# Kernel optimization log

Hardware: AMD Instinct MI355X
Metric: run time of the kernel (lower is better)

## Reference

```python
import jax, jax.numpy as jnp
import numpy as np

N, C_IN, C_OUT, K_CHEB, BATCH = 2048, 64, 64, 4, 8


def setup_inputs() -> dict:
    key = jax.random.key(0)
    k1, k2, k3, k4, k5 = jax.random.split(key, 5)
    # Xavier-uniform-like scales
    s_nn = float(np.sqrt(6.0 / (N + N)))
    s_th = float(np.sqrt(6.0 / (C_IN + C_OUT)))
    return {
        "X": jax.random.normal(k1, (BATCH, N, C_IN), dtype=jnp.float32),
        "Ws": jax.random.uniform(k2, (N, N), jnp.float32, -s_nn, s_nn),
        "W_alpha": jax.random.uniform(k3, (N, N), jnp.float32, -s_nn, s_nn),
        "Theta_s": jax.random.uniform(k4, (K_CHEB, C_IN, C_OUT), jnp.float32, -s_th, s_th),
        "Theta_d": jax.random.uniform(k5, (K_CHEB, C_IN, C_OUT), jnp.float32, -s_th, s_th),
    }


def reference(X, Ws, W_alpha, Theta_s, Theta_d):
    B, n, c_in = X.shape
    K = Theta_s.shape[0]

    # ---- static filter: sum_k (T_k(Ws) @ X) @ Theta_s[k] ----
    # T_0 = I, so T_0 @ X = X
    static_filter = jnp.einsum('bni,io->bno', X, Theta_s[0])
    if K > 1:
        T_prev2 = jnp.eye(n, dtype=X.dtype)
        T_prev1 = Ws  # T_1
        for k in range(1, K):
            TkX = jnp.einsum('nm,bmi->bni', T_prev1, X)
            static_filter = static_filter + jnp.einsum('bni,io->bno', TkX, Theta_s[k])
            if k + 1 < K:  # incremental Chebyshev recursion (same values as from-scratch)
                T_prev2, T_prev1 = T_prev1, 2.0 * (Ws @ T_prev1) - T_prev2

    # ---- dynamic filter ----
    # Wd = X @ (W_alpha @ X)^T  -> [B, n, n]
    WaX = jnp.einsum('nm,bmi->bni', W_alpha, X)
    Wd = jnp.einsum('bni,bmi->bnm', X, WaX)

    dynamic_filter = jnp.einsum('bni,io->bno', X, Theta_d[0])
    if K > 1:
        Td_prev2 = jnp.broadcast_to(jnp.eye(n, dtype=X.dtype), (B, n, n))
        Td_prev1 = Wd  # T_1
        for k in range(1, K):
            TkX = jnp.einsum('bnm,bmi->bni', Td_prev1, X)
            dynamic_filter = dynamic_filter + jnp.einsum('bni,io->bno', TkX, Theta_d[k])
            if k + 1 < K:
                Td_prev2, Td_prev1 = Td_prev1, 2.0 * jnp.matmul(Wd, Td_prev1) - Td_prev2

    return jax.nn.relu(static_filter) + jax.nn.relu(dynamic_filter)
```

## Files before the change

### kernel.cpp

```cpp
#include <hip/hip_runtime.h>

typedef __attribute__((ext_vector_type(8))) short bf16x8;
typedef __attribute__((ext_vector_type(4))) float f32x4;

__device__ __forceinline__ ushort f32_to_bf16(float f) {
    union { float f; unsigned u; } v; v.f = f;
    unsigned b = v.u + 0x7FFF + ((v.u >> 16) & 1);
    return (ushort)(b >> 16);
}
__device__ __forceinline__ float bf16_to_f32(ushort h) {
    union { unsigned u; float f; } v; v.u = ((unsigned)h) << 16;
    return v.f;
}
__device__ __forceinline__ void split2(float x, ushort& a, ushort& b) {
    a = f32_to_bf16(x); float r1 = x - bf16_to_f32(a);
    b = f32_to_bf16(r1);
}

__device__ __forceinline__ void vmwait4() { asm volatile("s_waitcnt vmcnt(4)" ::: "memory"); }
__device__ __forceinline__ void vmwait0() { asm volatile("s_waitcnt vmcnt(0)" ::: "memory"); }
__device__ __forceinline__ void lgwait0() { asm volatile("s_waitcnt lgkmcnt(0)" ::: "memory"); }
__device__ __forceinline__ void blockbar() {
    __builtin_amdgcn_sched_barrier(0);
    __builtin_amdgcn_s_barrier();
    __builtin_amdgcn_sched_barrier(0);
}

__device__ __forceinline__ void stage64x64(const ushort* gsrc, int row_stride_elems,
                                           char* lds, int t256) {
    const char* gb = (const char*)gsrc;
    const int rs = row_stride_elems * 2;
#pragma unroll
    for (int j = 0; j < 2; ++j) {
        int o = (j * 256 + t256) * 16;
        int row = o >> 7;
        int col = (o & 127) ^ ((row & 7) << 4);
        __builtin_amdgcn_global_load_lds(
            (const __attribute__((address_space(1))) unsigned int*)(gb + row * rs + col),
            (__attribute__((address_space(3))) unsigned int*)(lds + o), 16, 0, 0);
    }
}

__device__ __forceinline__ bf16x8 fragld(const char* lds, int row, int kbyte) {
    return *(const bf16x8*)(lds + (row << 7) + (kbyte ^ ((row & 7) << 4)));
}

__global__ __launch_bounds__(256) void prep_all(const float* __restrict__ X,
        ushort* __restrict__ XT1, ushort* __restrict__ XT2,
        ushort* __restrict__ X1o, ushort* __restrict__ X2o,
        const float* __restrict__ Ws, ushort* __restrict__ Ws16,
        const float* __restrict__ Wa, ushort* __restrict__ Wa1,
        const float* __restrict__ Ths, ushort* __restrict__ ThsT) {
    __shared__ float tile[64][68];
    const int bx = blockIdx.x;
    const int t = threadIdx.x;
    if (bx < 256) {
        const int b = bx >> 5, n0 = (bx & 31) * 64;
#pragma unroll
        for (int it = 0; it < 4; ++it) {
            int f = it * 256 + t, r = f >> 4, q = (f & 15) * 4;
            float4 v = *(const float4*)&X[((size_t)b * 2048 + n0 + r) * 64 + q];
            tile[r][q + 0] = v.x; tile[r][q + 1] = v.y; tile[r][q + 2] = v.z; tile[r][q + 3] = v.w;
        }
        __syncthreads();
#pragma unroll
        for (int it = 0; it < 4; ++it) {
            int f = it * 256 + t, c = f >> 4, q = (f & 15) * 4;
            ushort4 h1, h2;
            split2(tile[q + 0][c], h1.x, h2.x); split2(tile[q + 1][c], h1.y, h2.y);
            split2(tile[q + 2][c], h1.z, h2.z); split2(tile[q + 3][c], h1.w, h2.w);
            size_t a = (size_t)(b * 64 + c) * 2048 + n0 + q;
            *(ushort4*)&XT1[a] = h1; *(ushort4*)&XT2[a] = h2;
        }
#pragma unroll
        for (int it = 0; it < 4; ++it) {
            int f = it * 256 + t, n = f >> 4, q = (f & 15) * 4;
            ushort4 h1, h2;
            split2(tile[n][q + 0], h1.x, h2.x); split2(tile[n][q + 1], h1.y, h2.y);
            split2(tile[n][q + 2], h1.z, h2.z); split2(tile[n][q + 3], h1.w, h2.w);
            size_t a = (size_t)(n0 + n) * 512 + b * 64 + q;
            *(ushort4*)&X1o[a] = h1; *(ushort4*)&X2o[a] = h2;
        }
    } else if (bx < 2304) {
        size_t idx = ((size_t)(bx - 256) * 256 + t) * 8;
#pragma unroll
        for (int h = 0; h < 2; ++h) {
            float4 v = *(const float4*)&Ws[idx + h * 4];
            ushort4 a;
            a.x = f32_to_bf16(v.x); a.y = f32_to_bf16(v.y);
            a.z = f32_to_bf16(v.z); a.w = f32_to_bf16(v.w);
            *(ushort4*)&Ws16[idx + h * 4] = a;
        }
    } else if (bx < 4352) {
        size_t idx = ((size_t)(bx - 2304) * 256 + t) * 8;
#pragma unroll
        for (int h = 0; h < 2; ++h) {
            float4 v = *(const float4*)&Wa[idx + h * 4];
            ushort4 a;
            a.x = f32_to_bf16(v.x); a.y = f32_to_bf16(v.y);
            a.z = f32_to_bf16(v.z); a.w = f32_to_bf16(v.w);
            *(ushort4*)&Wa1[idx + h * 4] = a;
        }
    } else {
        int idx = (bx - 4352) * 256 + t;
        int k = idx >> 12, o = (idx >> 6) & 63, i = idx & 63;
        ThsT[idx] = f32_to_bf16(Ths[k * 4096 + i * 64 + o]);
    }
}

template <int MODE>
__device__ __forceinline__ void gemm_s_body(int bx, const ushort* __restrict__ A,
        const ushort* __restrict__ BT, const ushort* __restrict__ CinT,
        ushort* __restrict__ YT, ushort* __restrict__ Yo, char* ls) {
    const int t = threadIdx.x;
    const int g = t >> 8, t256 = t & 255;
    const int m0 = (bx & 31) * 64, c0 = (bx >> 5) * 64;
    const int lane = t & 63;
    const int wg = (t >> 6) & 3, wr = wg >> 1, wc = wg & 1;
    const int l15 = lane & 15, l4 = lane >> 4;
    char* base = ls + g * 32768;
    const ushort* Ap = A + (size_t)m0 * 2048 + (size_t)g * 1024;
    const ushort* Bp = BT + (size_t)c0 * 2048 + (size_t)g * 1024;

    f32x4 z = {0.f, 0.f, 0.f, 0.f};
    f32x4 acc[2][2];
    acc[0][0] = z; acc[0][1] = z; acc[1][0] = z; acc[1][1] = z;

    stage64x64(Ap, 2048, base, t256);
    stage64x64(Bp, 2048, base + 8192, t256);
    for (int ts = 0; ts < 16; ++ts) {
        char* cur = base + (ts & 1) * 16384;
        if (ts < 15) {
            char* nxt = base + ((ts + 1) & 1) * 16384;
            stage64x64(Ap + (ts + 1) * 64, 2048, nxt, t256);
            stage64x64(Bp + (ts + 1) * 64, 2048, nxt + 8192, t256);
            vmwait4();
        } else {
            vmwait0();
        }
        blockbar();
#pragma unroll
        for (int s = 0; s < 2; ++s) {
            const int kb = s * 64 + l4 * 16;
            bf16x8 aF[2], bF[2];
#pragma unroll
            for (int f = 0; f < 2; ++f) {
                aF[f] = fragld(cur, wr * 32 + f * 16 + l15, kb);
                bF[f] = fragld(cur + 8192, wc * 32 + f * 16 + l15, kb);
            }
#pragma unroll
            for (int i = 0; i < 2; ++i)
#pragma unroll
                for (int j = 0; j < 2; ++j)
                    acc[i][j] = __builtin_amdgcn_mfma_f32_16x16x32_bf16(aF[i], bF[j], acc[i][j], 0, 0, 0);
        }
        lgwait0();
        blockbar();
    }

    float* red = (float*)ls;
    ushort* tileo = (ushort*)(ls + 17408);
    if (g == 0) {
#pragma unroll
        for (int i = 0; i < 2; ++i)
#pragma unroll
            for (int j = 0; j < 2; ++j) {
                const int lrb = wr * 32 + i * 16 + l4 * 4;
                const int lc = wc * 32 + j * 16 + l15;
#pragma unroll
                for (int r = 0; r < 4; ++r) red[(lrb + r) * 65 + lc] = acc[i][j][r];
            }
    }
    __syncthreads();
    if (g == 1) {
#pragma unroll
        for (int i = 0; i < 2; ++i)
#pragma unroll
            for (int j = 0; j < 2; ++j) {
                const int lrb = wr * 32 + i * 16 + l4 * 4;
                const int lc = wc * 32 + j * 16 + l15;
                float vv[4];
#pragma unroll
                for (int r = 0; r < 4; ++r) vv[r] = red[(lrb + r) * 65 + lc] + acc[i][j][r];
                if (MODE == 1) {
                    ushort4 ci = *(const ushort4*)&CinT[(size_t)(c0 + lc) * 2048 + m0 + lrb];
                    vv[0] = 2.f * vv[0] - bf16_to_f32(ci.x);
                    vv[1] = 2.f * vv[1] - bf16_to_f32(ci.y);
                    vv[2] = 2.f * vv[2] - bf16_to_f32(ci.z);
                    vv[3] = 2.f * vv[3] - bf16_to_f32(ci.w);
                }
                ushort4 p;
                p.x = f32_to_bf16(vv[0]); p.y = f32_to_bf16(vv[1]);
                p.z = f32_to_bf16(vv[2]); p.w = f32_to_bf16(vv[3]);
                *(ushort4*)&YT[(size_t)(c0 + lc) * 2048 + m0 + lrb] = p;
                tileo[(lrb + 0) * 64 + lc] = p.x;
                tileo[(lrb + 1) * 64 + lc] = p.y;
                tileo[(lrb + 2) * 64 + lc] = p.z;
                tileo[(lrb + 3) * 64 + lc] = p.w;
            }
    }
    __syncthreads();
    {
        int row = t >> 3, ch = t & 7;
        *(uint4*)&Yo[(size_t)(m0 + row) * 512 + c0 + ch * 8] = *(uint4*)&tileo[row * 64 + ch * 8];
    }
}

__device__ __forceinline__ void gemm3_body(int bx, const ushort* __restrict__ A1,
        const ushort* __restrict__ B1, const ushort* __restrict__ B2,
        float* __restrict__ WaXT, char* ls) {
    const int t = threadIdx.x;
    const int g = t >> 8, t256 = t & 255;
    const int m0 = (bx & 31) * 64, c0 = (bx >> 5) * 64;
    const int lane = t & 63;
    const int wg = (t >> 6) & 3, wr = wg >> 1, wc = wg & 1;
    const int l15 = lane & 15, l4 = lane >> 4;
    char* base = ls + g * 24576;
    const size_t kbase = (size_t)g * 1024;

    f32x4 z = {0.f, 0.f, 0.f, 0.f};
    f32x4 acc[2][2];
    acc[0][0] = z; acc[0][1] = z; acc[1][0] = z; acc[1][1] = z;

    for (int k0 = 0; k0 < 1024; k0 += 64) {
        stage64x64(A1 + (size_t)m0 * 2048 + kbase + k0, 2048, base + 0 * 8192, t256);
        stage64x64(B1 + (size_t)c0 * 2048 + kbase + k0, 2048, base + 1 * 8192, t256);
        stage64x64(B2 + (size_t)c0 * 2048 + kbase + k0, 2048, base + 2 * 8192, t256);
        __syncthreads();
#pragma unroll
        for (int s = 0; s < 2; ++s) {
            const int kb = s * 64 + l4 * 16;
            bf16x8 a1F[2], b1F[2], b2F[2];
#pragma unroll
            for (int f = 0; f < 2; ++f) {
                const int ar = wr * 32 + f * 16 + l15;
                const int br = wc * 32 + f * 16 + l15;
                a1F[f] = fragld(base + 0 * 8192, ar, kb);
                b1F[f] = fragld(base + 1 * 8192, br, kb);
                b2F[f] = fragld(base + 2 * 8192, br, kb);
            }
#pragma unroll
            for (int i = 0; i < 2; ++i)
#pragma unroll
                for (int j = 0; j < 2; ++j) {
                    f32x4 a = acc[i][j];
                    a = __builtin_amdgcn_mfma_f32_16x16x32_bf16(a1F[i], b1F[j], a, 0, 0, 0);
                    a = __builtin_amdgcn_mfma_f32_16x16x32_bf16(a1F[i], b2F[j], a, 0, 0, 0);
                    acc[i][j] = a;
                }
        }
        __syncthreads();
    }

    float* red = (float*)ls;
    if (g == 0) {
#pragma unroll
        for (int i = 0; i < 2; ++i)
#pragma unroll
            for (int j = 0; j < 2; ++j) {
                const int lrb = wr * 32 + i * 16 + l4 * 4;
                const int lc = wc * 32 + j * 16 + l15;
#pragma unroll
                for (int r = 0; r < 4; ++r) red[(lrb + r) * 65 + lc] = acc[i][j][r];
            }
    }
    __syncthreads();
    if (g == 1) {
#pragma unroll
        for (int i = 0; i < 2; ++i)
#pragma unroll
            for (int j = 0; j < 2; ++j) {
                const int lrb = wr * 32 + i * 16 + l4 * 4;
                const int lc = wc * 32 + j * 16 + l15;
                f32x4 v;
#pragma unroll
                for (int r = 0; r < 4; ++r) v[r] = red[(lrb + r) * 65 + lc] + acc[i][j][r];
                *(f32x4*)&WaXT[(size_t)(c0 + lc) * 2048 + m0 + lrb] = v;
            }
    }
}

__device__ __forceinline__ void gram_body(int bx, const float* __restrict__ WaXT,
        const ushort* __restrict__ XT1, const ushort* __restrict__ XT2,
        float* __restrict__ Gpart, char* lsraw) {
    const int b = bx & 7, chunk = bx >> 3;
    float (*Lw)[68] = (float(*)[68])lsraw;
    float (*Rx)[68] = (float(*)[68])(lsraw + 64 * 68 * 4);
    const int t = threadIdx.x;
    const int n0 = chunk * 64;
    {
        const int r = t >> 3, q = (t & 7) * 8;
        size_t a = (size_t)(b * 64 + r) * 2048 + n0 + q;
        *(float4*)&Lw[r][q]     = *(const float4*)&WaXT[a];
        *(float4*)&Lw[r][q + 4] = *(const float4*)&WaXT[a + 4];
#pragma unroll
        for (int h = 0; h < 2; ++h) {
            ushort4 h1 = *(const ushort4*)&XT1[a + h * 4];
            ushort4 h2 = *(const ushort4*)&XT2[a + h * 4];
            Rx[r][q + h * 4 + 0] = bf16_to_f32(h1.x) + bf16_to_f32(h2.x);
            Rx[r][q + h * 4 + 1] = bf16_to_f32(h1.y) + bf16_to_f32(h2.y);
            Rx[r][q + h * 4 + 2] = bf16_to_f32(h1.z) + bf16_to_f32(h2.z);
            Rx[r][q + h * 4 + 3] = bf16_to_f32(h1.w) + bf16_to_f32(h2.w);
        }
    }
    __syncthreads();
    if (t < 256) {
        const int tx = t & 15, ty = t >> 4;
        float acc[4][4] = {{0.f,0.f,0.f,0.f},{0.f,0.f,0.f,0.f},{0.f,0.f,0.f,0.f},{0.f,0.f,0.f,0.f}};
        for (int n = 0; n < 64; ++n) {
            float a[4], bb[4];
#pragma unroll
            for (int i = 0; i < 4; ++i) { a[i] = Lw[ty * 4 + i][n]; bb[i] = Rx[tx * 4 + i][n]; }
#pragma unroll
            for (int i = 0; i < 4; ++i)
#pragma unroll
                for (int j = 0; j < 4; ++j) acc[i][j] = fmaf(a[i], bb[j], acc[i][j]);
        }
        float* gp = Gpart + (size_t)(chunk * 8 + b) * 4096;
#pragma unroll
        for (int i = 0; i < 4; ++i)
            *(float4*)&gp[(ty * 4 + i) * 64 + tx * 4] =
                make_float4(acc[i][0], acc[i][1], acc[i][2], acc[i][3]);
    }
}

__device__ __forceinline__ void cheb_body(int b, const float* __restrict__ Gpart,
        const float* __restrict__ Thd, ushort* __restrict__ DT1, ushort* __restrict__ DT2,
        char* lsraw) {
    float (*Gs)[68]  = (float(*)[68])lsraw;
    float (*C2s)[68] = (float(*)[68])(lsraw + 17408);
    float (*C3s)[68] = (float(*)[68])(lsraw + 34816);
    const int t = threadIdx.x;
    for (int i = t; i < 4096; i += 512) {
        float s = 0.f;
#pragma unroll
        for (int c = 0; c < 32; ++c) s += Gpart[((size_t)c * 8 + b) * 4096 + i];
        Gs[i >> 6][i & 63] = s;
    }
    __syncthreads();
    const int tx = t & 15, ty = (t >> 4) & 15;
    const int r0 = ty * 4, c0 = tx * 4;
    const bool act = t < 256;

    if (act) {
        float p[4][4] = {{0,0,0,0},{0,0,0,0},{0,0,0,0},{0,0,0,0}};
        for (int k = 0; k < 64; ++k) {
            float ar[4] = {Gs[r0][k], Gs[r0+1][k], Gs[r0+2][k], Gs[r0+3][k]};
            float4 bv = *(const float4*)&Gs[k][c0];
            float br[4] = {bv.x, bv.y, bv.z, bv.w};
#pragma unroll
            for (int i = 0; i < 4; ++i)
#pragma unroll
                for (int j = 0; j < 4; ++j) p[i][j] = fmaf(ar[i], br[j], p[i][j]);
        }
#pragma unroll
        for (int i = 0; i < 4; ++i)
#pragma unroll
            for (int j = 0; j < 4; ++j)
                C2s[r0+i][c0+j] = 2.f * p[i][j] - ((r0+i) == (c0+j) ? 1.f : 0.f);
    }
    __syncthreads();
    if (act) {
        float q[4][4] = {{0,0,0,0},{0,0,0,0},{0,0,0,0},{0,0,0,0}};
        for (int k = 0; k < 64; ++k) {
            float ar[4] = {Gs[r0][k], Gs[r0+1][k], Gs[r0+2][k], Gs[r0+3][k]};
            float4 bv = *(const float4*)&C2s[k][c0];
            float br[4] = {bv.x, bv.y, bv.z, bv.w};
#pragma unroll
            for (int i = 0; i < 4; ++i)
#pragma unroll
                for (int j = 0; j < 4; ++j) q[i][j] = fmaf(ar[i], br[j], q[i][j]);
        }
#pragma unroll
        for (int i = 0; i < 4; ++i)
#pragma unroll
            for (int j = 0; j < 4; ++j)
                C3s[r0+i][c0+j] = 2.f * q[i][j] - Gs[r0+i][c0+j];
    }
    __syncthreads();
    float d[4][4];
    if (act) {
#pragma unroll
        for (int i = 0; i < 4; ++i) {
            float4 t0 = *(const float4*)&Thd[(r0+i) * 64 + c0];
            d[i][0] = t0.x; d[i][1] = t0.y; d[i][2] = t0.z; d[i][3] = t0.w;
        }
        for (int k = 0; k < 64; ++k) {
            float4 t1 = *(const float4*)&Thd[4096 + k * 64 + c0];
            float4 t2 = *(const float4*)&Thd[8192 + k * 64 + c0];
            float4 t3 = *(const float4*)&Thd[12288 + k * 64 + c0];
            float a1[4] = {Gs[r0][k], Gs[r0+1][k], Gs[r0+2][k], Gs[r0+3][k]};
            float a2[4] = {C2s[r0][k], C2s[r0+1][k], C2s[r0+2][k], C2s[r0+3][k]};
            float a3[4] = {C3s[r0][k], C3s[r0+1][k], C3s[r0+2][k], C3s[r0+3][k]};
            float b1[4] = {t1.x, t1.y, t1.z, t1.w};
            float b2[4] = {t2.x, t2.y, t2.z, t2.w};
            float b3[4] = {t3.x, t3.y, t3.z, t3.w};
#pragma unroll
            for (int i = 0; i < 4; ++i)
#pragma unroll
                for (int j = 0; j < 4; ++j) {
                    d[i][j] = fmaf(a1[i], b1[j], d[i][j]);
                    d[i][j] = fmaf(a2[i], b2[j], d[i][j]);
                    d[i][j] = fmaf(a3[i], b3[j], d[i][j]);
                }
        }
    }
    __syncthreads();
    if (act) {
#pragma unroll
        for (int i = 0; i < 4; ++i)
#pragma unroll
            for (int j = 0; j < 4; ++j) Gs[r0 + i][c0 + j] = d[i][j];
    }
    __syncthreads();
    for (int it = 0; it < 8; ++it) {
        int idx = it * 512 + t;
        int o = idx >> 6, ii = idx & 63;
        ushort h1, h2;
        split2(Gs[ii][o], h1, h2);
        DT1[b * 4096 + idx] = h1;
        DT2[b * 4096 + idx] = h2;
    }
}

__global__ __launch_bounds__(512, 4) void mega1(const ushort* __restrict__ Wa1,
        const ushort* __restrict__ XT1, const ushort* __restrict__ XT2,
        float* __restrict__ WaXT,
        const ushort* __restrict__ Ws16, ushort* __restrict__ Y1T, ushort* __restrict__ Y1o) {
    __shared__ __align__(16) char ls[65536];
    const int bx = blockIdx.x;
    if (bx < 256) gemm3_body(bx, Wa1, XT1, XT2, WaXT, ls);
    else          gemm_s_body<0>(bx - 256, Ws16, XT1, nullptr, Y1T, Y1o, ls);
}

__global__ __launch_bounds__(512, 4) void mega2(const ushort* __restrict__ Ws16,
        const ushort* __restrict__ Y1T, const ushort* __restrict__ XT1,
        ushort* __restrict__ Y2T, ushort* __restrict__ Y2o,
        const float* __restrict__ WaXT, const ushort* __restrict__ XT2,
        float* __restrict__ Gpart) {
    __shared__ __align__(16) char ls[65536];
    const int bx = blockIdx.x;
    if (bx < 256) gemm_s_body<1>(bx, Ws16, Y1T, XT1, Y2T, Y2o, ls);
    else          gram_body(bx - 256, WaXT, XT1, XT2, Gpart, ls);
}

__global__ __launch_bounds__(512, 4) void mega3(const ushort* __restrict__ Ws16,
        const ushort* __restrict__ Y2T, const ushort* __restrict__ Y1T,
        ushort* __restrict__ Y3T, ushort* __restrict__ Y3o,
        const float* __restrict__ Gpart, const float* __restrict__ Thd,
        ushort* __restrict__ DT1, ushort* __restrict__ DT2) {
    __shared__ __align__(16) char ls[65536];
    const int bx = blockIdx.x;
    if (bx < 256) gemm_s_body<1>(bx, Ws16, Y2T, Y1T, Y3T, Y3o, ls);
    else          cheb_body(bx - 256, Gpart, Thd, DT1, DT2, ls);
}

__global__ __launch_bounds__(256) void ep_fused(const ushort* __restrict__ ThsT,
                                                const ushort* __restrict__ DT1, const ushort* __restrict__ DT2,
                                                const ushort* __restrict__ X1o, const ushort* __restrict__ X2o,
                                                const ushort* __restrict__ Y1o, const ushort* __restrict__ Y2o,
                                                const ushort* __restrict__ Y3o,
                                                float* __restrict__ out) {
    __shared__ __align__(16) char ls[65536];
    const int b = blockIdx.y, n0 = blockIdx.x * 64;
    const int t = threadIdx.x, lane = t & 63, w = t >> 6, wr = w >> 1, wc = w & 1;
    const int l15 = lane & 15, l4 = lane >> 4;
    stage64x64(X1o + (size_t)n0 * 512 + b * 64, 512, ls + 0 * 8192, t);
    stage64x64(Y1o + (size_t)n0 * 512 + b * 64, 512, ls + 1 * 8192, t);
    stage64x64(Y2o + (size_t)n0 * 512 + b * 64, 512, ls + 2 * 8192, t);
    stage64x64(Y3o + (size_t)n0 * 512 + b * 64, 512, ls + 3 * 8192, t);
    stage64x64(ThsT + 0 * 4096, 64, ls + 4 * 8192, t);
    stage64x64(ThsT + 1 * 4096, 64, ls + 5 * 8192, t);
    stage64x64(ThsT + 2 * 4096, 64, ls + 6 * 8192, t);
    stage64x64(ThsT + 3 * 4096, 64, ls + 7 * 8192, t);
    __syncthreads();
    f32x4 z = {0.f, 0.f, 0.f, 0.f};
    f32x4 as[2][2], ad[2][2];
    as[0][0] = z; as[0][1] = z; as[1][0] = z; as[1][1] = z;
    ad[0][0] = z; ad[0][1] = z; ad[1][0] = z; ad[1][1] = z;
#pragma unroll
    for (int s = 0; s < 2; ++s) {
        const int kb = s * 64 + l4 * 16;
#pragma unroll
        for (int p = 0; p < 4; ++p) {
            bf16x8 aF[2], bF[2];
#pragma unroll
            for (int f = 0; f < 2; ++f) {
                aF[f] = fragld(ls + (4 + p) * 8192, wr * 32 + f * 16 + l15, kb);
                bF[f] = fragld(ls + p * 8192, wc * 32 + f * 16 + l15, kb);
            }
#pragma unroll
            for (int i = 0; i < 2; ++i)
#pragma unroll
                for (int j = 0; j < 2; ++j)
                    as[i][j] = __builtin_amdgcn_mfma_f32_16x16x32_bf16(aF[i], bF[j], as[i][j], 0, 0, 0);
        }
    }
    __syncthreads();
    stage64x64(DT1 + b * 4096, 64, ls + 1 * 8192, t);
    stage64x64(DT2 + b * 4096, 64, ls + 2 * 8192, t);
    stage64x64(X2o + (size_t)n0 * 512 + b * 64, 512, ls + 3 * 8192, t);
    __syncthreads();
#pragma unroll
    for (int s = 0; s < 2; ++s) {
        const int kb = s * 64 + l4 * 16;
        bf16x8 a1[2], a2[2], b0[2], b3[2];
#pragma unroll
        for (int f = 0; f < 2; ++f) {
            a1[f] = fragld(ls + 1 * 8192, wr * 32 + f * 16 + l15, kb);
            a2[f] = fragld(ls + 2 * 8192, wr * 32 + f * 16 + l15, kb);
            b0[f] = fragld(ls + 0 * 8192, wc * 32 + f * 16 + l15, kb);
            b3[f] = fragld(ls + 3 * 8192, wc * 32 + f * 16 + l15, kb);
        }
#pragma unroll
        for (int i = 0; i < 2; ++i)
#pragma unroll
            for (int j = 0; j < 2; ++j) {
                f32x4 a = ad[i][j];
                a = __builtin_amdgcn_mfma_f32_16x16x32_bf16(a1[i], b0[j], a, 0, 0, 0);
                a = __builtin_amdgcn_mfma_f32_16x16x32_bf16(a1[i], b3[j], a, 0, 0, 0);
                a = __builtin_amdgcn_mfma_f32_16x16x32_bf16(a2[i], b0[j], a, 0, 0, 0);
                ad[i][j] = a;
            }
    }
#pragma unroll
    for (int i = 0; i < 2; ++i)
#pragma unroll
        for (int j = 0; j < 2; ++j) {
            const int ob = wr * 32 + i * 16 + l4 * 4;
            const int nn = wc * 32 + j * 16 + l15;
            float4 o4;
            o4.x = fmaxf(as[i][j][0], 0.f) + fmaxf(ad[i][j][0], 0.f);
            o4.y = fmaxf(as[i][j][1], 0.f) + fmaxf(ad[i][j][1], 0.f);
            o4.z = fmaxf(as[i][j][2], 0.f) + fmaxf(ad[i][j][2], 0.f);
            o4.w = fmaxf(as[i][j][3], 0.f) + fmaxf(ad[i][j][3], 0.f);
            *(float4*)&out[((size_t)b * 2048 + n0 + nn) * 64 + ob] = o4;
        }
}

extern "C" void kernel_launch(void* const* d_in, const int* in_sizes, int n_in,
                              void* d_out, int out_size, void* d_ws, size_t ws_size,
                              hipStream_t stream) {
    (void)in_sizes; (void)n_in; (void)out_size;
    const float* X   = (const float*)d_in[0];
    const float* Ws  = (const float*)d_in[1];
    const float* Wa  = (const float*)d_in[2];
    const float* Ths = (const float*)d_in[3];
    const float* Thd = (const float*)d_in[4];

    char* p = (char*)d_ws;
    auto alloc = [&](size_t bytes) { char* r = p; p += (bytes + 255) & ~(size_t)255; return r; };
    ushort* XT1 = (ushort*)alloc(512ull * 2048 * 2);
    ushort* XT2 = (ushort*)alloc(512ull * 2048 * 2);
    ushort* X1o = (ushort*)alloc(2048ull * 512 * 2);
    ushort* X2o = (ushort*)alloc(2048ull * 512 * 2);
    ushort* Ws16 = (ushort*)alloc(2048ull * 2048 * 2);
    ushort* Wa1 = (ushort*)alloc(2048ull * 2048 * 2);
    ushort* Y1T = (ushort*)alloc(512ull * 2048 * 2);
    ushort* Y2T = (ushort*)alloc(512ull * 2048 * 2);
    ushort* Y3T = (ushort*)alloc(512ull * 2048 * 2);
    ushort* Y1o = (ushort*)alloc(2048ull * 512 * 2);
    ushort* Y2o = (ushort*)alloc(2048ull * 512 * 2);
    ushort* Y3o = (ushort*)alloc(2048ull * 512 * 2);
    float*  Gpart = (float*)alloc(32ull * 8 * 4096 * 4);
    ushort* DT1 = (ushort*)alloc(8ull * 4096 * 2);
    ushort* DT2 = (ushort*)alloc(8ull * 4096 * 2);
    ushort* ThsT = (ushort*)alloc(4ull * 4096 * 2);
    if ((size_t)(p - (char*)d_ws) > ws_size) return;
    float* WaXT = (float*)d_out;

    prep_all<<<4416, 256, 0, stream>>>(X, XT1, XT2, X1o, X2o, Ws, Ws16, Wa, Wa1, Ths, ThsT);
    mega1<<<512, 512, 0, stream>>>(Wa1, XT1, XT2, WaXT, Ws16, Y1T, Y1o);
    mega2<<<512, 512, 0, stream>>>(Ws16, Y1T, XT1, Y2T, Y2o, WaXT, XT2, Gpart);
    mega3<<<264, 512, 0, stream>>>(Ws16, Y2T, Y1T, Y3T, Y3o, Gpart, Thd, DT1, DT2);
    ep_fused<<<dim3(32, 8), 256, 0, stream>>>(ThsT, DT1, DT2, X1o, X2o, Y1o, Y2o, Y3o, (float*)d_out);
}
```

Before: 82.66 us.

## Restructure GEMM blocks to 256 threads with per-wave split-K over 128-wide tiles

The GEMM bodies move from 512-thread blocks (two 256-thread K-halves with 2x2 warp tiles) to 256-thread blocks. Each of the four waves owns a 64-wide K slice of a 128-wide staged tile and computes the full 64x64 output with 4x4 MFMA accumulators. A three-way LDS reduction merges the partial sums, and the gram and cheb helpers are adapted to the smaller block size. This aims to raise fragment reuse per LDS load and cut barrier overhead, at the cost of more accumulator registers per wave and a larger reduction step.

Result: slower. 87.85 us (+6.3%).

```diff
diff --git a/kernel.cpp b/kernel.cpp
--- a/kernel.cpp
+++ b/kernel.cpp
@@ -17,7 +17,7 @@
     b = f32_to_bf16(r1);
 }
 
-__device__ __forceinline__ void vmwait4() { asm volatile("s_waitcnt vmcnt(4)" ::: "memory"); }
+__device__ __forceinline__ void vmwait8() { asm volatile("s_waitcnt vmcnt(8)" ::: "memory"); }
 __device__ __forceinline__ void vmwait0() { asm volatile("s_waitcnt vmcnt(0)" ::: "memory"); }
 __device__ __forceinline__ void lgwait0() { asm volatile("s_waitcnt lgkmcnt(0)" ::: "memory"); }
 __device__ __forceinline__ void blockbar() {
@@ -40,9 +40,24 @@
             (__attribute__((address_space(3))) unsigned int*)(lds + o), 16, 0, 0);
     }
 }
-
 __device__ __forceinline__ bf16x8 fragld(const char* lds, int row, int kbyte) {
     return *(const bf16x8*)(lds + (row << 7) + (kbyte ^ ((row & 7) << 4)));
+}
+
+__device__ __forceinline__ void stage64x128(const ushort* gsrc, char* lds, int t) {
+    const char* gb = (const char*)gsrc;
+#pragma unroll
+    for (int j = 0; j < 4; ++j) {
+        int o = (j * 256 + t) * 16;
+        int row = o >> 8;
+        int col = (o & 255) ^ ((row & 7) << 4);
+        __builtin_amdgcn_global_load_lds(
+            (const __attribute__((address_space(1))) unsigned int*)(gb + row * 4096 + col),
+            (__attribute__((address_space(3))) unsigned int*)(lds + o), 16, 0, 0);
+    }
+}
+__device__ __forceinline__ bf16x8 fragld256(const char* lds, int row, int kbyte) {
+    return *(const bf16x8*)(lds + (row << 8) + (kbyte ^ ((row & 7) << 4)));
 }
 
 __global__ __launch_bounds__(256) void prep_all(const float* __restrict__ X,
@@ -109,81 +124,79 @@
 }
 
 template <int MODE>
-__device__ __forceinline__ void gemm_s_body(int bx, const ushort* __restrict__ A,
+__device__ __forceinline__ void gemm_sv2(int bx, const ushort* __restrict__ A,
         const ushort* __restrict__ BT, const ushort* __restrict__ CinT,
         ushort* __restrict__ YT, ushort* __restrict__ Yo, char* ls) {
     const int t = threadIdx.x;
-    const int g = t >> 8, t256 = t & 255;
     const int m0 = (bx & 31) * 64, c0 = (bx >> 5) * 64;
-    const int lane = t & 63;
-    const int wg = (t >> 6) & 3, wr = wg >> 1, wc = wg & 1;
-    const int l15 = lane & 15, l4 = lane >> 4;
-    char* base = ls + g * 32768;
-    const ushort* Ap = A + (size_t)m0 * 2048 + (size_t)g * 1024;
-    const ushort* Bp = BT + (size_t)c0 * 2048 + (size_t)g * 1024;
+    const int w = t >> 6, lane = t & 63, l15 = lane & 15, l4 = lane >> 4;
+    const int kb = w * 64 + l4 * 16;
+    const ushort* Ap = A + (size_t)m0 * 2048;
+    const ushort* Bp = BT + (size_t)c0 * 2048;
 
     f32x4 z = {0.f, 0.f, 0.f, 0.f};
-    f32x4 acc[2][2];
-    acc[0][0] = z; acc[0][1] = z; acc[1][0] = z; acc[1][1] = z;
-
-    stage64x64(Ap, 2048, base, t256);
-    stage64x64(Bp, 2048, base + 8192, t256);
+    f32x4 acc[4][4];
+#pragma unroll
+    for (int i = 0; i < 4; ++i)
+#pragma unroll
+        for (int j = 0; j < 4; ++j) acc[i][j] = z;
+
+    stage64x128(Ap, ls, t);
+    stage64x128(Bp, ls + 16384, t);
     for (int ts = 0; ts < 16; ++ts) {
-        char* cur = base + (ts & 1) * 16384;
+        char* cur = ls + (ts & 1) * 32768;
         if (ts < 15) {
-            char* nxt = base + ((ts + 1) & 1) * 16384;
-            stage64x64(Ap + (ts + 1) * 64, 2048, nxt, t256);
-            stage64x64(Bp + (ts + 1) * 64, 2048, nxt + 8192, t256);
-            vmwait4();
+            char* nxt = ls + ((ts + 1) & 1) * 32768;
+            stage64x128(Ap + (ts + 1) * 128, nxt, t);
+            stage64x128(Bp + (ts + 1) * 128, nxt + 16384, t);
+            vmwait8();
         } else {
             vmwait0();
         }
         blockbar();
-#pragma unroll
-        for (int s = 0; s < 2; ++s) {
-            const int kb = s * 64 + l4 * 16;
-            bf16x8 aF[2], bF[2];
-#pragma unroll
-            for (int f = 0; f < 2; ++f) {
-                aF[f] = fragld(cur, wr * 32 + f * 16 + l15, kb);
-                bF[f] = fragld(cur + 8192, wc * 32 + f * 16 + l15, kb);
-            }
-#pragma unroll
-            for (int i = 0; i < 2; ++i)
-#pragma unroll
-                for (int j = 0; j < 2; ++j)
-                    acc[i][j] = __builtin_amdgcn_mfma_f32_16x16x32_bf16(aF[i], bF[j], acc[i][j], 0, 0, 0);
-        }
+        bf16x8 aF[4], bF[4];
+#pragma unroll
+        for (int i = 0; i < 4; ++i) aF[i] = fragld256(cur, i * 16 + l15, kb);
+#pragma unroll
+        for (int j = 0; j < 4; ++j) bF[j] = fragld256(cur + 16384, j * 16 + l15, kb);
+#pragma unroll
+        for (int i = 0; i < 4; ++i)
+#pragma unroll
+            for (int j = 0; j < 4; ++j)
+                acc[i][j] = __builtin_amdgcn_mfma_f32_16x16x32_bf16(aF[i], bF[j], acc[i][j], 0, 0, 0);
         lgwait0();
         blockbar();
     }
 
     float* red = (float*)ls;
-    ushort* tileo = (ushort*)(ls + 17408);
-    if (g == 0) {
-#pragma unroll
-        for (int i = 0; i < 2; ++i)
-#pragma unroll
-            for (int j = 0; j < 2; ++j) {
-                const int lrb = wr * 32 + i * 16 + l4 * 4;
-                const int lc = wc * 32 + j * 16 + l15;
-#pragma unroll
-                for (int r = 0; r < 4; ++r) red[(lrb + r) * 65 + lc] = acc[i][j][r];
-            }
-    }
-    __syncthreads();
-    if (g == 1) {
-#pragma unroll
-        for (int i = 0; i < 2; ++i)
-#pragma unroll
-            for (int j = 0; j < 2; ++j) {
-                const int lrb = wr * 32 + i * 16 + l4 * 4;
-                const int lc = wc * 32 + j * 16 + l15;
+    ushort* tileo = (ushort*)(ls + 50176);
+    if (w < 3) {
+#pragma unroll
+        for (int i = 0; i < 4; ++i)
+#pragma unroll
+            for (int j = 0; j < 4; ++j) {
+                const int row = i * 16 + l4 * 4;
+                const int col = j * 16 + l15;
+#pragma unroll
+                for (int r = 0; r < 4; ++r) red[w * 4160 + (row + r) * 65 + col] = acc[i][j][r];
+            }
+    }
+    __syncthreads();
+    if (w == 3) {
+#pragma unroll
+        for (int i = 0; i < 4; ++i)
+#pragma unroll
+            for (int j = 0; j < 4; ++j) {
+                const int row = i * 16 + l4 * 4;
+                const int col = j * 16 + l15;
                 float vv[4];
 #pragma unroll
-                for (int r = 0; r < 4; ++r) vv[r] = red[(lrb + r) * 65 + lc] + acc[i][j][r];
+                for (int r = 0; r < 4; ++r) {
+                    const int rr = (row + r) * 65 + col;
+                    vv[r] = acc[i][j][r] + red[rr] + red[4160 + rr] + red[8320 + rr];
+                }
                 if (MODE == 1) {
-                    ushort4 ci = *(const ushort4*)&CinT[(size_t)(c0 + lc) * 2048 + m0 + lrb];
+                    ushort4 ci = *(const ushort4*)&CinT[(size_t)(c0 + col) * 2048 + m0 + row];
                     vv[0] = 2.f * vv[0] - bf16_to_f32(ci.x);
                     vv[1] = 2.f * vv[1] - bf16_to_f32(ci.y);
                     vv[2] = 2.f * vv[2] - bf16_to_f32(ci.z);
@@ -192,109 +205,106 @@
                 ushort4 p;
                 p.x = f32_to_bf16(vv[0]); p.y = f32_to_bf16(vv[1]);
                 p.z = f32_to_bf16(vv[2]); p.w = f32_to_bf16(vv[3]);
-                *(ushort4*)&YT[(size_t)(c0 + lc) * 2048 + m0 + lrb] = p;
-                tileo[(lrb + 0) * 64 + lc] = p.x;
-                tileo[(lrb + 1) * 64 + lc] = p.y;
-                tileo[(lrb + 2) * 64 + lc] = p.z;
-                tileo[(lrb + 3) * 64 + lc] = p.w;
-            }
-    }
-    __syncthreads();
-    {
-        int row = t >> 3, ch = t & 7;
+                *(ushort4*)&YT[(size_t)(c0 + col) * 2048 + m0 + row] = p;
+                tileo[(row + 0) * 64 + col] = p.x;
+                tileo[(row + 1) * 64 + col] = p.y;
+                tileo[(row + 2) * 64 + col] = p.z;
+                tileo[(row + 3) * 64 + col] = p.w;
+            }
+    }
+    __syncthreads();
+#pragma unroll
+    for (int it = 0; it < 2; ++it) {
+        int f = it * 256 + t;
+        int row = f >> 3, ch = f & 7;
         *(uint4*)&Yo[(size_t)(m0 + row) * 512 + c0 + ch * 8] = *(uint4*)&tileo[row * 64 + ch * 8];
     }
 }
 
-__device__ __forceinline__ void gemm3_body(int bx, const ushort* __restrict__ A1,
+__device__ __forceinline__ void gemm3v2(int bx, const ushort* __restrict__ A1,
         const ushort* __restrict__ B1, const ushort* __restrict__ B2,
         float* __restrict__ WaXT, char* ls) {
     const int t = threadIdx.x;
-    const int g = t >> 8, t256 = t & 255;
     const int m0 = (bx & 31) * 64, c0 = (bx >> 5) * 64;
-    const int lane = t & 63;
-    const int wg = (t >> 6) & 3, wr = wg >> 1, wc = wg & 1;
-    const int l15 = lane & 15, l4 = lane >> 4;
-    char* base = ls + g * 24576;
-    const size_t kbase = (size_t)g * 1024;
+    const int w = t >> 6, lane = t & 63, l15 = lane & 15, l4 = lane >> 4;
+    const int kb = w * 64 + l4 * 16;
 
     f32x4 z = {0.f, 0.f, 0.f, 0.f};
-    f32x4 acc[2][2];
-    acc[0][0] = z; acc[0][1] = z; acc[1][0] = z; acc[1][1] = z;
-
-    for (int k0 = 0; k0 < 1024; k0 += 64) {
-        stage64x64(A1 + (size_t)m0 * 2048 + kbase + k0, 2048, base + 0 * 8192, t256);
-        stage64x64(B1 + (size_t)c0 * 2048 + kbase + k0, 2048, base + 1 * 8192, t256);
-        stage64x64(B2 + (size_t)c0 * 2048 + kbase + k0, 2048, base + 2 * 8192, t256);
+    f32x4 acc[4][4];
+#pragma unroll
+    for (int i = 0; i < 4; ++i)
+#pragma unroll
+        for (int j = 0; j < 4; ++j) acc[i][j] = z;
+
+    for (int k0 = 0; k0 < 2048; k0 += 128) {
+        stage64x128(A1 + (size_t)m0 * 2048 + k0, ls, t);
+        stage64x128(B1 + (size_t)c0 * 2048 + k0, ls + 16384, t);
+        stage64x128(B2 + (size_t)c0 * 2048 + k0, ls + 32768, t);
         __syncthreads();
-#pragma unroll
-        for (int s = 0; s < 2; ++s) {
-            const int kb = s * 64 + l4 * 16;
-            bf16x8 a1F[2], b1F[2], b2F[2];
-#pragma unroll
-            for (int f = 0; f < 2; ++f) {
-                const int ar = wr * 32 + f * 16 + l15;
-                const int br = wc * 32 + f * 16 + l15;
-                a1F[f] = fragld(base + 0 * 8192, ar, kb);
-                b1F[f] = fragld(base + 1 * 8192, br, kb);
-                b2F[f] = fragld(base + 2 * 8192, br, kb);
-            }
-#pragma unroll
-            for (int i = 0; i < 2; ++i)
-#pragma unroll
-                for (int j = 0; j < 2; ++j) {
-                    f32x4 a = acc[i][j];
-                    a = __builtin_amdgcn_mfma_f32_16x16x32_bf16(a1F[i], b1F[j], a, 0, 0, 0);
-                    a = __builtin_amdgcn_mfma_f32_16x16x32_bf16(a1F[i], b2F[j], a, 0, 0, 0);
-                    acc[i][j] = a;
+        bf16x8 aF[4], b1F[4], b2F[4];
+#pragma unroll
+        for (int i = 0; i < 4; ++i) {
+            aF[i]  = fragld256(ls, i * 16 + l15, kb);
+            b1F[i] = fragld256(ls + 16384, i * 16 + l15, kb);
+            b2F[i] = fragld256(ls + 32768, i * 16 + l15, kb);
+        }
+#pragma unroll
+        for (int i = 0; i < 4; ++i)
+#pragma unroll
+            for (int j = 0; j < 4; ++j) {
+                f32x4 a = acc[i][j];
+                a = __builtin_amdgcn_mfma_f32_16x16x32_bf16(aF[i], b1F[j], a, 0, 0, 0);
+                a = __builtin_amdgcn_mfma_f32_16x16x32_bf16(aF[i], b2F[j], a, 0, 0, 0);
+                acc[i][j] = a;
+            }
+        __syncthreads();
+    }
+
+    float* red = (float*)ls;
+    if (w < 3) {
+#pragma unroll
+        for (int i = 0; i < 4; ++i)
+#pragma unroll
+            for (int j = 0; j < 4; ++j) {
+                const int row = i * 16 + l4 * 4;
+                const int col = j * 16 + l15;
+#pragma unroll
+                for (int r = 0; r < 4; ++r) red[w * 4160 + (row + r) * 65 + col] = acc[i][j][r];
+            }
+    }
+    __syncthreads();
+    if (w == 3) {
+#pragma unroll
+        for (int i = 0; i < 4; ++i)
+#pragma unroll
+            for (int j = 0; j < 4; ++j) {
+                const int row = i * 16 + l4 * 4;
+                const int col = j * 16 + l15;
+                f32x4 v;
+#pragma unroll
+                for (int r = 0; r < 4; ++r) {
+                    const int rr = (row + r) * 65 + col;
+                    v[r] = acc[i][j][r] + red[rr] + red[4160 + rr] + red[8320 + rr];
                 }
-        }
-        __syncthreads();
-    }
-
-    float* red = (float*)ls;
-    if (g == 0) {
-#pragma unroll
-        for (int i = 0; i < 2; ++i)
-#pragma unroll
-            for (int j = 0; j < 2; ++j) {
-                const int lrb = wr * 32 + i * 16 + l4 * 4;
-                const int lc = wc * 32 + j * 16 + l15;
-#pragma unroll
-                for (int r = 0; r < 4; ++r) red[(lrb + r) * 65 + lc] = acc[i][j][r];
-            }
-    }
-    __syncthreads();
-    if (g == 1) {
-#pragma unroll
-        for (int i = 0; i < 2; ++i)
-#pragma unroll
-            for (int j = 0; j < 2; ++j) {
-                const int lrb = wr * 32 + i * 16 + l4 * 4;
-                const int lc = wc * 32 + j * 16 + l15;
-                f32x4 v;
-#pragma unroll
-                for (int r = 0; r < 4; ++r) v[r] = red[(lrb + r) * 65 + lc] + acc[i][j][r];
-                *(f32x4*)&WaXT[(size_t)(c0 + lc) * 2048 + m0 + lrb] = v;
-            }
-    }
-}
-
-__device__ __forceinline__ void gram_body(int bx, const float* __restrict__ WaXT,
+                *(f32x4*)&WaXT[(size_t)(c0 + col) * 2048 + m0 + row] = v;
+            }
+    }
+}
+
+__device__ __forceinline__ void gramv2(int bx, const float* __restrict__ WaXT,
         const ushort* __restrict__ XT1, const ushort* __restrict__ XT2,
         float* __restrict__ Gpart, char* lsraw) {
     const int b = bx & 7, chunk = bx >> 3;
     float (*Lw)[68] = (float(*)[68])lsraw;
-    float (*Rx)[68] = (float(*)[68])(lsraw + 64 * 68 * 4);
+    float (*Rx)[68] = (float(*)[68])(lsraw + 17408);
     const int t = threadIdx.x;
     const int n0 = chunk * 64;
     {
-        const int r = t >> 3, q = (t & 7) * 8;
+        const int r = t >> 2, q = (t & 3) * 16;
         size_t a = (size_t)(b * 64 + r) * 2048 + n0 + q;
-        *(float4*)&Lw[r][q]     = *(const float4*)&WaXT[a];
-        *(float4*)&Lw[r][q + 4] = *(const float4*)&WaXT[a + 4];
-#pragma unroll
-        for (int h = 0; h < 2; ++h) {
+#pragma unroll
+        for (int h = 0; h < 4; ++h) {
+            *(float4*)&Lw[r][q + h * 4] = *(const float4*)&WaXT[a + h * 4];
             ushort4 h1 = *(const ushort4*)&XT1[a + h * 4];
             ushort4 h2 = *(const ushort4*)&XT2[a + h * 4];
             Rx[r][q + h * 4 + 0] = bf16_to_f32(h1.x) + bf16_to_f32(h2.x);
@@ -304,7 +314,7 @@
         }
     }
     __syncthreads();
-    if (t < 256) {
+    {
         const int tx = t & 15, ty = t >> 4;
         float acc[4][4] = {{0.f,0.f,0.f,0.f},{0.f,0.f,0.f,0.f},{0.f,0.f,0.f,0.f},{0.f,0.f,0.f,0.f}};
         for (int n = 0; n < 64; ++n) {
@@ -324,25 +334,24 @@
     }
 }
 
-__device__ __forceinline__ void cheb_body(int b, const float* __restrict__ Gpart,
+__device__ __forceinline__ void chebv2(int b, const float* __restrict__ Gpart,
         const float* __restrict__ Thd, ushort* __restrict__ DT1, ushort* __restrict__ DT2,
         char* lsraw) {
     float (*Gs)[68]  = (float(*)[68])lsraw;
     float (*C2s)[68] = (float(*)[68])(lsraw + 17408);
     float (*C3s)[68] = (float(*)[68])(lsraw + 34816);
     const int t = threadIdx.x;
-    for (int i = t; i < 4096; i += 512) {
+    for (int i = t; i < 4096; i += 256) {
         float s = 0.f;
 #pragma unroll
         for (int c = 0; c < 32; ++c) s += Gpart[((size_t)c * 8 + b) * 4096 + i];
         Gs[i >> 6][i & 63] = s;
     }
     __syncthreads();
-    const int tx = t & 15, ty = (t >> 4) & 15;
+    const int tx = t & 15, ty = t >> 4;
     const int r0 = ty * 4, c0 = tx * 4;
-    const bool act = t < 256;
-
-    if (act) {
+
+    {
         float p[4][4] = {{0,0,0,0},{0,0,0,0},{0,0,0,0},{0,0,0,0}};
         for (int k = 0; k < 64; ++k) {
             float ar[4] = {Gs[r0][k], Gs[r0+1][k], Gs[r0+2][k], Gs[r0+3][k]};
@@ -360,7 +369,7 @@
                 C2s[r0+i][c0+j] = 2.f * p[i][j] - ((r0+i) == (c0+j) ? 1.f : 0.f);
     }
     __syncthreads();
-    if (act) {
+    {
         float q[4][4] = {{0,0,0,0},{0,0,0,0},{0,0,0,0},{0,0,0,0}};
         for (int k = 0; k < 64; ++k) {
             float ar[4] = {Gs[r0][k], Gs[r0+1][k], Gs[r0+2][k], Gs[r0+3][k]};
@@ -379,7 +388,7 @@
     }
     __syncthreads();
     float d[4][4];
-    if (act) {
+    {
 #pragma unroll
         for (int i = 0; i < 4; ++i) {
             float4 t0 = *(const float4*)&Thd[(r0+i) * 64 + c0];
@@ -406,15 +415,14 @@
         }
     }
     __syncthreads();
-    if (act) {
-#pragma unroll
-        for (int i = 0; i < 4; ++i)
-#pragma unroll
-            for (int j = 0; j < 4; ++j) Gs[r0 + i][c0 + j] = d[i][j];
-    }
-    __syncthreads();
-    for (int it = 0; it < 8; ++it) {
-        int idx = it * 512 + t;
+#pragma unroll
+    for (int i = 0; i < 4; ++i)
+#pragma unroll
+        for (int j = 0; j < 4; ++j) Gs[r0 + i][c0 + j] = d[i][j];
+    __syncthreads();
+#pragma unroll
+    for (int it = 0; it < 16; ++it) {
+        int idx = it * 256 + t;
         int o = idx >> 6, ii = idx & 63;
         ushort h1, h2;
         split2(Gs[ii][o], h1, h2);
@@ -423,36 +431,36 @@
     }
 }
 
-__global__ __launch_bounds__(512, 4) void mega1(const ushort* __restrict__ Wa1,
+__global__ __launch_bounds__(256, 2) void mega1(const ushort* __restrict__ Wa1,
         const ushort* __restrict__ XT1, const ushort* __restrict__ XT2,
         float* __restrict__ WaXT,
         const ushort* __restrict__ Ws16, ushort* __restrict__ Y1T, ushort* __restrict__ Y1o) {
     __shared__ __align__(16) char ls[65536];
     const int bx = blockIdx.x;
-    if (bx < 256) gemm3_body(bx, Wa1, XT1, XT2, WaXT, ls);
-    else          gemm_s_body<0>(bx - 256, Ws16, XT1, nullptr, Y1T, Y1o, ls);
-}
-
-__global__ __launch_bounds__(512, 4) void mega2(const ushort* __restrict__ Ws16,
+    if (bx < 256) gemm3v2(bx, Wa1, XT1, XT2, WaXT, ls);
+    else          gemm_sv2<0>(bx - 256, Ws16, XT1, nullptr, Y1T, Y1o, ls);
+}
+
+__global__ __launch_bounds__(256, 2) void mega2(const ushort* __restrict__ Ws16,
         const ushort* __restrict__ Y1T, const ushort* __restrict__ XT1,
         ushort* __restrict__ Y2T, ushort* __restrict__ Y2o,
         const float* __restrict__ WaXT, const ushort* __restrict__ XT2,
         float* __restrict__ Gpart) {
     __shared__ __align__(16) char ls[65536];
     const int bx = blockIdx.x;
-    if (bx < 256) gemm_s_body<1>(bx, Ws16, Y1T, XT1, Y2T, Y2o, ls);
-    else          gram_body(bx - 256, WaXT, XT1, XT2, Gpart, ls);
-}
-
-__global__ __launch_bounds__(512, 4) void mega3(const ushort* __restrict__ Ws16,
+    if (bx < 256) gemm_sv2<1>(bx, Ws16, Y1T, XT1, Y2T, Y2o, ls);
+    else          gramv2(bx - 256, WaXT, XT1, XT2, Gpart, ls);
+}
+
+__global__ __launch_bounds__(256, 2) void mega3(const ushort* __restrict__ Ws16,
         const ushort* __restrict__ Y2T, const ushort* __restrict__ Y1T,
         ushort* __restrict__ Y3T, ushort* __restrict__ Y3o,
         const float* __restrict__ Gpart, const float* __restrict__ Thd,
         ushort* __restrict__ DT1, ushort* __restrict__ DT2) {
     __shared__ __align__(16) char ls[65536];
     const int bx = blockIdx.x;
-    if (bx < 256) gemm_s_body<1>(bx, Ws16, Y2T, Y1T, Y3T, Y3o, ls);
-    else          cheb_body(bx - 256, Gpart, Thd, DT1, DT2, ls);
+    if (bx < 256) gemm_sv2<1>(bx, Ws16, Y2T, Y1T, Y3T, Y3o, ls);
+    else          chebv2(bx - 256, Gpart, Thd, DT1, DT2, ls);
 }
 
 __global__ __launch_bounds__(256) void ep_fused(const ushort* __restrict__ ThsT,
@@ -570,8 +578,8 @@
     float* WaXT = (float*)d_out;
 
     prep_all<<<4416, 256, 0, stream>>>(X, XT1, XT2, X1o, X2o, Ws, Ws16, Wa, Wa1, Ths, ThsT);
-    mega1<<<512, 512, 0, stream>>>(Wa1, XT1, XT2, WaXT, Ws16, Y1T, Y1o);
-    mega2<<<512, 512, 0, stream>>>(Ws16, Y1T, XT1, Y2T, Y2o, WaXT, XT2, Gpart);
-    mega3<<<264, 512, 0, stream>>>(Ws16, Y2T, Y1T, Y3T, Y3o, Gpart, Thd, DT1, DT2);
+    mega1<<<512, 256, 0, stream>>>(Wa1, XT1, XT2, WaXT, Ws16, Y1T, Y1o);
+    mega2<<<512, 256, 0, stream>>>(Ws16, Y1T, XT1, Y2T, Y2o, WaXT, XT2, Gpart);
+    mega3<<<264, 256, 0, stream>>>(Ws16, Y2T, Y1T, Y3T, Y3o, Gpart, Thd, DT1, DT2);
     ep_fused<<<dim3(32, 8), 256, 0, stream>>>(ThsT, DT1, DT2, X1o, X2o, Y1o, Y2o, Y3o, (float*)d_out);
 }
```
